# Performance work log

Measured on AMD Instinct MI355X. Metric: run time of the kernel, lower is better.

Reference implementation:

```python
import jax, jax.numpy as jnp
import numpy as np

B, S, D_IN, D_OUT = 4, 2048, 1024, 1024


def setup_inputs() -> dict:
    key = jax.random.key(0)
    k1, k2, k3, k4 = jax.random.split(key, 4)
    scale = 1.0 / np.sqrt(D_IN)
    return {
        "x": jax.random.normal(k1, (B, S, D_IN), dtype=jnp.float32),
        "W_q": jax.random.normal(k2, (D_OUT, D_IN), dtype=jnp.float32) * scale,
        "W_k": jax.random.normal(k3, (D_OUT, D_IN), dtype=jnp.float32) * scale,
        "W_v": jax.random.normal(k4, (D_OUT, D_IN), dtype=jnp.float32) * scale,
    }


def reference(x, W_q, W_k, W_v):
    # torch nn.Linear: y = x @ W.T (bias=False)
    q = jnp.einsum("bsd,od->bso", x, W_q)
    k = jnp.einsum("bsd,od->bso", x, W_k)
    v = jnp.einsum("bsd,od->bso", x, W_v)
    s = q.shape[1]
    scores = jnp.einsum("bqo,bko->bqk", q, k)  # [B, S, S]
    causal = jnp.triu(jnp.ones((s, s), dtype=bool), k=1)
    scores = jnp.where(causal, -jnp.inf, scores)
    inv_sqrt_d = 1.0 / jnp.sqrt(jnp.asarray(q.shape[-1], scores.dtype))
    attn = jax.nn.softmax(scores * inv_sqrt_d, axis=-1)
    # dropout p=0.0 -> identity (deterministic reference)
    return jnp.einsum("bqk,bko->bqo", attn, v)
```

## Files before the change

kernel.cpp:

```cpp
#include <hip/hip_runtime.h>

typedef unsigned short u16;
typedef __bf16 bf16x8 __attribute__((ext_vector_type(8)));
typedef float f32x4 __attribute__((ext_vector_type(4)));

#define AS1 __attribute__((address_space(1)))
#define AS3 __attribute__((address_space(3)))

__device__ inline u16 f2bf(float f) {
  union { float f; unsigned u; } a; a.f = f;
  unsigned u = a.u;
  return (u16)((u + 0x7fffu + ((u >> 16) & 1u)) >> 16);
}

__global__ __launch_bounds__(256) void cvt_kernel(const float* __restrict__ in,
                                                  u16* __restrict__ out) {
  size_t i = ((size_t)blockIdx.x * 256 + threadIdx.x) * 4;
  float4 v = *(const float4*)(in + i);
  ushort4 o;
  o.x = f2bf(v.x); o.y = f2bf(v.y); o.z = f2bf(v.z); o.w = f2bf(v.w);
  *(ushort4*)(out + i) = o;
}

__global__ __launch_bounds__(256) void cvt3_kernel(
    const float* __restrict__ a, const float* __restrict__ b, const float* __restrict__ c,
    u16* __restrict__ oa, u16* __restrict__ ob, u16* __restrict__ oc) {
  int bid = blockIdx.x;
  const float* in; u16* out;
  if (bid < 1024) { in = a; out = oa; }
  else if (bid < 2048) { in = b; out = ob; bid -= 1024; }
  else { in = c; out = oc; bid -= 2048; }
  size_t i = ((size_t)bid * 256 + threadIdx.x) * 4;
  float4 v = *(const float4*)(in + i);
  ushort4 o;
  o.x = f2bf(v.x); o.y = f2bf(v.y); o.z = f2bf(v.z); o.w = f2bf(v.w);
  *(ushort4*)(out + i) = o;
}

template <typename CT, int BM>
__device__ __forceinline__ void gemm_core(
    const u16* __restrict__ A, const u16* __restrict__ B, CT* __restrict__ C,
    int nt, int lda, int ldb, int ldc, int m0, int n0, bool atom) {
  constexpr int ABUF = BM * 64;
  constexpr int ASW = BM / 64;
  constexpr int PH_MI = BM / 128;
  __shared__ __align__(16) u16 lds[2 * ABUF + 32768];

  const int tid = threadIdx.x;
  const int ln = tid & 63, wv = tid >> 6;
  const int wr = wv >> 2, wc = wv & 3;

  auto sweep = [&](const u16* src, int ld, int t, int s, int base) {
    const int c = s * 512 + tid;
    const int row = c >> 3, slot = c & 7;
    const int col = (slot ^ (row & 7)) * 8;
    __builtin_amdgcn_global_load_lds(
        (const AS1 void*)(src + (size_t)row * ld + (size_t)t * 64 + col),
        (AS3 void*)(&lds[base + c * 8]), 16, 0, 0);
  };

  f32x4 acc[2 * BM / 64][4] = {};

#pragma unroll
  for (int s = 0; s < 4; ++s) sweep(B, ldb, 0, s, 2 * ABUF);
#pragma unroll
  for (int s = 0; s < ASW; ++s) sweep(A, lda, 0, s, 0);
  if (nt > 1) {
#pragma unroll
    for (int s = 0; s < 4; ++s) sweep(B, ldb, 1, s, 2 * ABUF + 16384);
#pragma unroll
    for (int s = 0; s < ASW; ++s) sweep(A, lda, 1, s, ABUF);
    if constexpr (ASW == 4) asm volatile("s_waitcnt vmcnt(8)" ::: "memory");
    else                    asm volatile("s_waitcnt vmcnt(6)" ::: "memory");
  } else {
    asm volatile("s_waitcnt vmcnt(0)" ::: "memory");
  }
  __builtin_amdgcn_s_barrier();

  for (int t = 0; t < nt; ++t) {
    const int p = t & 1;
    const u16* La = &lds[p * ABUF];
    const u16* Lb = &lds[2 * ABUF + p * 16384];
    bf16x8 bfr[4][2];
#pragma unroll
    for (int q = 0; q < 4; ++q) {
      if (q == 0) {
        __builtin_amdgcn_sched_barrier(0);
#pragma unroll
        for (int ni = 0; ni < 4; ++ni)
#pragma unroll
          for (int ks = 0; ks < 2; ++ks) {
            const int row = wc * 64 + ni * 16 + (ln & 15);
            const int kc = ks * 4 + (ln >> 4);
            bfr[ni][ks] = *(const bf16x8*)&Lb[row * 64 + ((kc ^ (row & 7)) << 3)];
          }
      }
      bf16x8 afr[PH_MI][2];
#pragma unroll
      for (int mi = 0; mi < PH_MI; ++mi)
#pragma unroll
        for (int ks = 0; ks < 2; ++ks) {
          const int row = wr * (BM / 2) + (q * PH_MI + mi) * 16 + (ln & 15);
          const int kc = ks * 4 + (ln >> 4);
          afr[mi][ks] = *(const bf16x8*)&La[row * 64 + ((kc ^ (row & 7)) << 3)];
        }
      if constexpr (PH_MI == 2) {
        if (q == 0)      { if (t >= 1 && t + 1 < nt) { sweep(A, lda, t + 1, 0, (p ^ 1) * ABUF); sweep(A, lda, t + 1, 1, (p ^ 1) * ABUF); } }
        else if (q == 1) { if (t >= 1 && t + 1 < nt) { sweep(A, lda, t + 1, 2, (p ^ 1) * ABUF); sweep(A, lda, t + 1, 3, (p ^ 1) * ABUF); } }
        else if (q == 2) { if (t + 2 < nt) { sweep(B, ldb, t + 2, 0, 2 * ABUF + p * 16384); sweep(B, ldb, t + 2, 1, 2 * ABUF + p * 16384); } }
        else             { if (t + 2 < nt) { sweep(B, ldb, t + 2, 2, 2 * ABUF + p * 16384); sweep(B, ldb, t + 2, 3, 2 * ABUF + p * 16384); } }
      } else {
        if (q == 0)      { if (t >= 1 && t + 1 < nt) { sweep(A, lda, t + 1, 0, (p ^ 1) * ABUF); sweep(A, lda, t + 1, 1, (p ^ 1) * ABUF); } }
        else if (q == 2) { if (t + 2 < nt) { sweep(B, ldb, t + 2, 0, 2 * ABUF + p * 16384); sweep(B, ldb, t + 2, 1, 2 * ABUF + p * 16384); } }
        else if (q == 3) { if (t + 2 < nt) { sweep(B, ldb, t + 2, 2, 2 * ABUF + p * 16384); sweep(B, ldb, t + 2, 3, 2 * ABUF + p * 16384); } }
      }

      __builtin_amdgcn_s_barrier();
      __builtin_amdgcn_s_setprio(1);
#pragma unroll
      for (int mi = 0; mi < PH_MI; ++mi)
#pragma unroll
        for (int ni = 0; ni < 4; ++ni)
#pragma unroll
          for (int ks = 0; ks < 2; ++ks)
            acc[q * PH_MI + mi][ni] = __builtin_amdgcn_mfma_f32_16x16x32_bf16(
                afr[mi][ks], bfr[ni][ks], acc[q * PH_MI + mi][ni], 0, 0, 0);
      __builtin_amdgcn_s_setprio(0);
      if (q == 3) {
        if (t + 2 < nt)      asm volatile("s_waitcnt vmcnt(4)" ::: "memory");
        else if (t + 1 < nt) asm volatile("s_waitcnt vmcnt(0)" ::: "memory");
      }
      __builtin_amdgcn_s_barrier();
    }
  }

#pragma unroll
  for (int mi = 0; mi < 2 * BM / 64; ++mi) {
    const int rbase = m0 + wr * (BM / 2) + mi * 16 + (ln >> 4) * 4;
#pragma unroll
    for (int ni = 0; ni < 4; ++ni) {
      const int col = n0 + wc * 64 + ni * 16 + (ln & 15);
#pragma unroll
      for (int r = 0; r < 4; ++r) {
        const float v = acc[mi][ni][r];
        CT* ptr = &C[(size_t)(rbase + r) * ldc + col];
        if constexpr (sizeof(CT) == 4) {
          if (atom) atomicAdd((float*)ptr, v);
          else *(float*)ptr = v;
        } else {
          *ptr = f2bf(v);
        }
      }
    }
  }
}

__global__ __launch_bounds__(512, 2) void proj_qk_kernel(
    const u16* __restrict__ xb, const u16* __restrict__ wqb,
    const u16* __restrict__ wkb, u16* __restrict__ Qb, u16* __restrict__ Kb) {
  const int bid = blockIdx.x;
  const int w = bid >> 7, r = bid & 127;
  const int m0 = (r >> 2) * 256, n0 = (r & 3) * 256;
  const u16* B = w ? wkb : wqb;
  u16* C = w ? Kb : Qb;
  gemm_core<u16, 256>(xb + (size_t)m0 * 1024, B + (size_t)n0 * 1024, C,
                      16, 1024, 1024, 1024, m0, n0, false);
}

__global__ __launch_bounds__(512, 2) void vt_kernel(
    const u16* __restrict__ wvb, const u16* __restrict__ xb, u16* __restrict__ VTb) {
  const int z = blockIdx.x >> 6, r = blockIdx.x & 63;
  const int m0 = (r >> 3) * 128, n0 = (r & 7) * 256;
  gemm_core<u16, 128>(wvb + (size_t)m0 * 1024,
                      xb + (size_t)z * 2048 * 1024 + (size_t)n0 * 1024,
                      VTb + (size_t)z * 1024 * 2048,
                      16, 1024, 1024, 2048, m0, n0, false);
}

__global__ __launch_bounds__(512, 2) void qkt_kernel(
    const u16* __restrict__ Qb, const u16* __restrict__ Kb, float* __restrict__ Sb) {
  const int x = blockIdx.x;
  int mi = 0;
  while ((mi + 1) * (mi + 2) / 2 <= x) ++mi;
  const int ni = x - mi * (mi + 1) / 2;
  const int m0 = mi * 256, n0 = ni * 256;
  const u16* A = Qb + (size_t)blockIdx.y * 2048 * 1024 + (size_t)m0 * 1024;
  const u16* B = Kb + (size_t)blockIdx.y * 2048 * 1024 + (size_t)n0 * 1024;
  float* C = Sb + (size_t)blockIdx.y * 2048 * 2048;
  gemm_core<float, 256>(A, B, C, 16, 1024, 1024, 2048, m0, n0, false);
}

__global__ __launch_bounds__(512, 2) void pv_kernel(
    const u16* __restrict__ P, const u16* __restrict__ VTb, float* __restrict__ out) {
  const int c = blockIdx.x;
  int m, k0, ntc; bool atom;
  if (c < 4) { m = c; k0 = 0; ntc = 4 * (c + 1); atom = false; }
  else {
    const int j = c - 4;
    m = 4 + (j >> 1);
    const int nth = 2 * (m + 1);
    k0 = (j & 1) * nth; ntc = nth; atom = true;
  }
  const int m0 = m * 256, n0 = blockIdx.y * 256;
  const u16* A = P + (size_t)blockIdx.z * 2048 * 4096 + (size_t)m0 * 4096 + (size_t)k0 * 64;
  const u16* B = VTb + (size_t)blockIdx.z * 1024 * 2048 + (size_t)n0 * 2048 + (size_t)k0 * 64;
  float* C = out + (size_t)blockIdx.z * 2048 * 1024;
  gemm_core<float, 256>(A, B, C, ntc, 4096, 2048, 1024, m0, n0, atom);
}

__global__ __launch_bounds__(256) void softmax_kernel(float* __restrict__ S, float scale) {
  const int q = blockIdx.x;
  const bool full = (q >= 1024);
  float* row = S + ((size_t)blockIdx.y * 2048 + q) * 2048;
  const int t = threadIdx.x;
  float4 v0 = *(const float4*)(row + t * 4);
  float4 v1 = full ? *(const float4*)(row + 1024 + t * 4) : float4{0, 0, 0, 0};
  float x[8] = {v0.x, v0.y, v0.z, v0.w, v1.x, v1.y, v1.z, v1.w};
  float m = -3.4e38f;
#pragma unroll
  for (int i = 0; i < 8; ++i) {
    const int j = (i < 4) ? (t * 4 + i) : (1024 + t * 4 + (i - 4));
    x[i] = (j <= q) ? x[i] * scale : -3.4e38f;
    m = fmaxf(m, x[i]);
  }
#pragma unroll
  for (int off = 32; off > 0; off >>= 1) m = fmaxf(m, __shfl_xor(m, off, 64));
  __shared__ float redm[4], reds[4];
  const int ln = t & 63, wv = t >> 6;
  if (ln == 0) redm[wv] = m;
  __syncthreads();
  m = fmaxf(fmaxf(redm[0], redm[1]), fmaxf(redm[2], redm[3]));

  float p[8];
  float s = 0.f;
#pragma unroll
  for (int i = 0; i < 8; ++i) {
    p[i] = __expf(x[i] - m);
    s += p[i];
  }
#pragma unroll
  for (int off = 32; off > 0; off >>= 1) s += __shfl_xor(s, off, 64);
  if (ln == 0) reds[wv] = s;
  __syncthreads();
  s = reds[0] + reds[1] + reds[2] + reds[3];
  const float r = 1.0f / s;

  u16* prow = (u16*)row;
  ushort4 o0, o1;
  o0.x = f2bf(p[0] * r); o0.y = f2bf(p[1] * r); o0.z = f2bf(p[2] * r); o0.w = f2bf(p[3] * r);
  *(ushort4*)(prow + t * 4) = o0;
  if (full) {
    o1.x = f2bf(p[4] * r); o1.y = f2bf(p[5] * r); o1.z = f2bf(p[6] * r); o1.w = f2bf(p[7] * r);
    *(ushort4*)(prow + 1024 + t * 4) = o1;
  }
}

extern "C" void kernel_launch(void* const* d_in, const int* in_sizes, int n_in,
                              void* d_out, int out_size, void* d_ws, size_t ws_size,
                              hipStream_t stream) {
  const float* x  = (const float*)d_in[0];
  const float* Wq = (const float*)d_in[1];
  const float* Wk = (const float*)d_in[2];
  const float* Wv = (const float*)d_in[3];
  float* out = (float*)d_out;

  char* ws = (char*)d_ws;
  u16* xb   = (u16*)(ws);
  u16* wqb  = (u16*)(ws + (16ul << 20));
  u16* wkb  = (u16*)(ws + (18ul << 20));
  u16* wvb  = (u16*)(ws + (20ul << 20));
  u16* Qb   = (u16*)(ws + (22ul << 20));
  u16* Kb   = (u16*)(ws + (38ul << 20));
  u16* VTb  = (u16*)(ws + (54ul << 20));
  float* Sb = (float*)(ws + (70ul << 20));

  for (int b = 0; b < 4; ++b)
    hipMemsetAsync(out + ((size_t)b * 2048 + 1024) * 1024, 0, 1024 * 1024 * 4, stream);

  cvt_kernel<<<8192, 256, 0, stream>>>(x, xb);
  cvt3_kernel<<<3072, 256, 0, stream>>>(Wq, Wk, Wv, wqb, wkb, wvb);

  proj_qk_kernel<<<256, 512, 0, stream>>>(xb, wqb, wkb, Qb, Kb);
  vt_kernel<<<256, 512, 0, stream>>>(wvb, xb, VTb);

  qkt_kernel<<<dim3(36, 4), 512, 0, stream>>>(Qb, Kb, Sb);

  softmax_kernel<<<dim3(2048, 4), 256, 0, stream>>>(Sb, 0.03125f);

  pv_kernel<<<dim3(12, 4, 4), 512, 0, stream>>>((const u16*)Sb, VTb, out);
}
```

Baseline: 173.4 us.

## Merge launches, co-schedule V projection with QK^T, and replace atomics with split-K scratch reduce

Folds the x and weight conversions into one kernel, and runs the V-transpose projection in the same launch as the causal QK^T tiles so both fill the GPU together. It drops the memset and atomicAdd split-K in the PV GEMM in favour of a table-driven tile schedule, where the second half of each split writes to scratch and a separate reduce kernel adds it into the output. This removes launch overhead and atomic contention and improves wave balance, at the cost of an extra read/write pass over part of the output and a scratch buffer that reuses the xb workspace region (xb is dead by then).

```diff
diff --git a/kernel.cpp b/kernel.cpp
--- a/kernel.cpp
+++ b/kernel.cpp
@@ -13,23 +13,17 @@
   return (u16)((u + 0x7fffu + ((u >> 16) & 1u)) >> 16);
 }
 
-__global__ __launch_bounds__(256) void cvt_kernel(const float* __restrict__ in,
-                                                  u16* __restrict__ out) {
-  size_t i = ((size_t)blockIdx.x * 256 + threadIdx.x) * 4;
-  float4 v = *(const float4*)(in + i);
-  ushort4 o;
-  o.x = f2bf(v.x); o.y = f2bf(v.y); o.z = f2bf(v.z); o.w = f2bf(v.w);
-  *(ushort4*)(out + i) = o;
-}
-
-__global__ __launch_bounds__(256) void cvt3_kernel(
-    const float* __restrict__ a, const float* __restrict__ b, const float* __restrict__ c,
-    u16* __restrict__ oa, u16* __restrict__ ob, u16* __restrict__ oc) {
+__global__ __launch_bounds__(256) void cvt_all_kernel(
+    const float* __restrict__ x, const float* __restrict__ wq,
+    const float* __restrict__ wk, const float* __restrict__ wv,
+    u16* __restrict__ xb, u16* __restrict__ wqb,
+    u16* __restrict__ wkb, u16* __restrict__ wvb) {
   int bid = blockIdx.x;
   const float* in; u16* out;
-  if (bid < 1024) { in = a; out = oa; }
-  else if (bid < 2048) { in = b; out = ob; bid -= 1024; }
-  else { in = c; out = oc; bid -= 2048; }
+  if (bid < 8192) { in = x; out = xb; }
+  else if (bid < 9216) { in = wq; out = wqb; bid -= 8192; }
+  else if (bid < 10240) { in = wk; out = wkb; bid -= 9216; }
+  else { in = wv; out = wvb; bid -= 10240; }
   size_t i = ((size_t)bid * 256 + threadIdx.x) * 4;
   float4 v = *(const float4*)(in + i);
   ushort4 o;
@@ -39,12 +33,12 @@
 
 template <typename CT, int BM>
 __device__ __forceinline__ void gemm_core(
+    u16* __restrict__ lds,
     const u16* __restrict__ A, const u16* __restrict__ B, CT* __restrict__ C,
-    int nt, int lda, int ldb, int ldc, int m0, int n0, bool atom) {
+    int nt, int lda, int ldb, int ldc, int m0, int n0) {
   constexpr int ABUF = BM * 64;
   constexpr int ASW = BM / 64;
   constexpr int PH_MI = BM / 128;
-  __shared__ __align__(16) u16 lds[2 * ABUF + 32768];
 
   const int tid = threadIdx.x;
   const int ln = tid & 63, wv = tid >> 6;
@@ -144,12 +138,8 @@
       for (int r = 0; r < 4; ++r) {
         const float v = acc[mi][ni][r];
         CT* ptr = &C[(size_t)(rbase + r) * ldc + col];
-        if constexpr (sizeof(CT) == 4) {
-          if (atom) atomicAdd((float*)ptr, v);
-          else *(float*)ptr = v;
-        } else {
-          *ptr = f2bf(v);
-        }
+        if constexpr (sizeof(CT) == 4) *(float*)ptr = v;
+        else                           *ptr = f2bf(v);
       }
     }
   }
@@ -158,54 +148,72 @@
 __global__ __launch_bounds__(512, 2) void proj_qk_kernel(
     const u16* __restrict__ xb, const u16* __restrict__ wqb,
     const u16* __restrict__ wkb, u16* __restrict__ Qb, u16* __restrict__ Kb) {
+  __shared__ __align__(16) u16 lds[65536];
   const int bid = blockIdx.x;
   const int w = bid >> 7, r = bid & 127;
   const int m0 = (r >> 2) * 256, n0 = (r & 3) * 256;
   const u16* B = w ? wkb : wqb;
   u16* C = w ? Kb : Qb;
-  gemm_core<u16, 256>(xb + (size_t)m0 * 1024, B + (size_t)n0 * 1024, C,
-                      16, 1024, 1024, 1024, m0, n0, false);
-}
-
-__global__ __launch_bounds__(512, 2) void vt_kernel(
+  gemm_core<u16, 256>(lds, xb + (size_t)m0 * 1024, B + (size_t)n0 * 1024, C,
+                      16, 1024, 1024, 1024, m0, n0);
+}
+
+__global__ __launch_bounds__(512, 2) void vtqkt_kernel(
+    const u16* __restrict__ Qb, const u16* __restrict__ Kb, float* __restrict__ Sb,
     const u16* __restrict__ wvb, const u16* __restrict__ xb, u16* __restrict__ VTb) {
-  const int z = blockIdx.x >> 6, r = blockIdx.x & 63;
-  const int m0 = (r >> 3) * 128, n0 = (r & 7) * 256;
-  gemm_core<u16, 128>(wvb + (size_t)m0 * 1024,
-                      xb + (size_t)z * 2048 * 1024 + (size_t)n0 * 1024,
-                      VTb + (size_t)z * 1024 * 2048,
-                      16, 1024, 1024, 2048, m0, n0, false);
-}
-
-__global__ __launch_bounds__(512, 2) void qkt_kernel(
-    const u16* __restrict__ Qb, const u16* __restrict__ Kb, float* __restrict__ Sb) {
-  const int x = blockIdx.x;
-  int mi = 0;
-  while ((mi + 1) * (mi + 2) / 2 <= x) ++mi;
-  const int ni = x - mi * (mi + 1) / 2;
-  const int m0 = mi * 256, n0 = ni * 256;
-  const u16* A = Qb + (size_t)blockIdx.y * 2048 * 1024 + (size_t)m0 * 1024;
-  const u16* B = Kb + (size_t)blockIdx.y * 2048 * 1024 + (size_t)n0 * 1024;
-  float* C = Sb + (size_t)blockIdx.y * 2048 * 2048;
-  gemm_core<float, 256>(A, B, C, 16, 1024, 1024, 2048, m0, n0, false);
-}
+  __shared__ __align__(16) u16 lds[65536];
+  const int bid = blockIdx.x;
+  if (bid < 144) {
+    const int z = bid / 36, x = bid % 36;
+    int mi = 0;
+    while ((mi + 1) * (mi + 2) / 2 <= x) ++mi;
+    const int ni = x - mi * (mi + 1) / 2;
+    const int m0 = mi * 256, n0 = ni * 256;
+    const u16* A = Qb + (size_t)z * 2048 * 1024 + (size_t)m0 * 1024;
+    const u16* B = Kb + (size_t)z * 2048 * 1024 + (size_t)n0 * 1024;
+    float* C = Sb + (size_t)z * 2048 * 2048;
+    gemm_core<float, 256>(lds, A, B, C, 16, 1024, 1024, 2048, m0, n0);
+  } else {
+    int r = bid - 144;
+    const int z = r >> 6; r &= 63;
+    const int m0 = (r >> 3) * 128, n0 = (r & 7) * 256;
+    gemm_core<u16, 128>(lds, wvb + (size_t)m0 * 1024,
+                        xb + (size_t)z * 2048 * 1024 + (size_t)n0 * 1024,
+                        VTb + (size_t)z * 1024 * 2048,
+                        16, 1024, 1024, 2048, m0, n0);
+  }
+}
+
+__constant__ signed char PVM[13] = {7, 7, 6, 6, 5, 5, 4, 4, 3, 3, 2, 1, 0};
+__constant__ signed char PVK[13] = {0, 16, 0, 14, 0, 12, 0, 10, 0, 8, 0, 0, 0};
+__constant__ signed char PVN[13] = {16, 16, 14, 14, 12, 12, 10, 10, 8, 8, 12, 8, 4};
+__constant__ signed char PVS[13] = {0, 1, 0, 1, 0, 1, 0, 1, 0, 1, 0, 0, 0};
 
 __global__ __launch_bounds__(512, 2) void pv_kernel(
-    const u16* __restrict__ P, const u16* __restrict__ VTb, float* __restrict__ out) {
+    const u16* __restrict__ P, const u16* __restrict__ VTb,
+    float* __restrict__ out, float* __restrict__ scr) {
+  __shared__ __align__(16) u16 lds[65536];
   const int c = blockIdx.x;
-  int m, k0, ntc; bool atom;
-  if (c < 4) { m = c; k0 = 0; ntc = 4 * (c + 1); atom = false; }
-  else {
-    const int j = c - 4;
-    m = 4 + (j >> 1);
-    const int nth = 2 * (m + 1);
-    k0 = (j & 1) * nth; ntc = nth; atom = true;
-  }
+  const int m = PVM[c], k0 = PVK[c], ntc = PVN[c];
   const int m0 = m * 256, n0 = blockIdx.y * 256;
-  const u16* A = P + (size_t)blockIdx.z * 2048 * 4096 + (size_t)m0 * 4096 + (size_t)k0 * 64;
-  const u16* B = VTb + (size_t)blockIdx.z * 1024 * 2048 + (size_t)n0 * 2048 + (size_t)k0 * 64;
-  float* C = out + (size_t)blockIdx.z * 2048 * 1024;
-  gemm_core<float, 256>(A, B, C, ntc, 4096, 2048, 1024, m0, n0, atom);
+  const size_t z = blockIdx.z;
+  const u16* A = P + z * 2048 * 4096 + (size_t)m0 * 4096 + (size_t)k0 * 64;
+  const u16* B = VTb + z * 1024 * 2048 + (size_t)n0 * 2048 + (size_t)k0 * 64;
+  float* C = PVS[c] ? (scr + z * 1280 * 1024 - (size_t)768 * 1024)
+                    : (out + z * 2048 * 1024);
+  gemm_core<float, 256>(lds, A, B, C, ntc, 4096, 2048, 1024, m0, n0);
+}
+
+__global__ __launch_bounds__(256) void reduce_kernel(float* __restrict__ out,
+                                                     const float* __restrict__ scr) {
+  const size_t i = ((size_t)blockIdx.x * 256 + threadIdx.x) * 4;
+  const size_t zsz = 1280 * 1024;
+  const size_t z = i / zsz, rem = i - z * zsz;
+  float4 a = *(const float4*)(scr + i);
+  float4* o = (float4*)(out + z * 2048 * 1024 + (size_t)768 * 1024 + rem);
+  float4 b = *o;
+  b.x += a.x; b.y += a.y; b.z += a.z; b.w += a.w;
+  *o = b;
 }
 
 __global__ __launch_bounds__(256) void softmax_kernel(float* __restrict__ S, float scale) {
@@ -273,19 +281,17 @@
   u16* Kb   = (u16*)(ws + (38ul << 20));
   u16* VTb  = (u16*)(ws + (54ul << 20));
   float* Sb = (float*)(ws + (70ul << 20));
-
-  for (int b = 0; b < 4; ++b)
-    hipMemsetAsync(out + ((size_t)b * 2048 + 1024) * 1024, 0, 1024 * 1024 * 4, stream);
-
-  cvt_kernel<<<8192, 256, 0, stream>>>(x, xb);
-  cvt3_kernel<<<3072, 256, 0, stream>>>(Wq, Wk, Wv, wqb, wkb, wvb);
+  float* Osc = (float*)(ws);
+
+  cvt_all_kernel<<<11264, 256, 0, stream>>>(x, Wq, Wk, Wv, xb, wqb, wkb, wvb);
 
   proj_qk_kernel<<<256, 512, 0, stream>>>(xb, wqb, wkb, Qb, Kb);
-  vt_kernel<<<256, 512, 0, stream>>>(wvb, xb, VTb);
-
-  qkt_kernel<<<dim3(36, 4), 512, 0, stream>>>(Qb, Kb, Sb);
+
+  vtqkt_kernel<<<400, 512, 0, stream>>>(Qb, Kb, Sb, wvb, xb, VTb);
 
   softmax_kernel<<<dim3(2048, 4), 256, 0, stream>>>(Sb, 0.03125f);
 
-  pv_kernel<<<dim3(12, 4, 4), 512, 0, stream>>>((const u16*)Sb, VTb, out);
-}
+  pv_kernel<<<dim3(13, 4, 4), 512, 0, stream>>>((const u16*)Sb, VTb, out, Osc);
+
+  reduce_kernel<<<5120, 256, 0, stream>>>(out, Osc);
+}
```

Result: faster. 158.7 us (-8.5%).
